# Optimization experiments

Hardware: AMD Instinct MI355X
Metric: run time of the kernel (lower is better)

Reference implementation:

```python
import jax, jax.numpy as jnp
import numpy as np

NUM_EXPERTS = 8
TOP_K = 2


def setup_inputs() -> dict:
    key = jax.random.key(0)
    k1, k2, k3, k4, k5 = jax.random.split(key, 5)
    B, S, H, F, E = 4, 2048, 1024, 4096, NUM_EXPERTS
    return {
        "hidden_states": jax.random.normal(k1, (B, S, H), dtype=jnp.float32),
        "gate_w": jax.random.normal(k2, (E, H), dtype=jnp.float32) * 0.02,
        "w1": jax.random.normal(k3, (E, F, H), dtype=jnp.float32) * 0.02,
        "w3": jax.random.normal(k4, (E, F, H), dtype=jnp.float32) * 0.02,
        "w2": jax.random.normal(k5, (E, H, F), dtype=jnp.float32) * 0.02,
    }


def reference(hidden_states, gate_w, w1, w3, w2):
    B, S, H = hidden_states.shape
    E = gate_w.shape[0]
    x = hidden_states.reshape(-1, H)  # [T, H]
    T = x.shape[0]

    # Router: logits -> fp32 softmax -> top-k -> renormalize (Mixtral)
    router_logits = x @ gate_w.T  # [T, E]
    probs = jax.nn.softmax(router_logits.astype(jnp.float32), axis=-1)
    top_w, top_idx = jax.lax.top_k(probs, TOP_K)  # [T, K]
    top_w = top_w / jnp.sum(top_w, axis=-1, keepdims=True)
    top_w = top_w.astype(x.dtype)

    # Combine weights per (token, expert); zero for unselected experts.
    comb = jnp.zeros((T, E), dtype=x.dtype).at[
        jnp.arange(T)[:, None], top_idx
    ].add(top_w)  # [T, E]

    out = jnp.zeros((T, H), dtype=x.dtype)
    for e in range(E):  # structural loop over distinct expert weights
        h = jax.nn.silu(x @ w1[e].T) * (x @ w3[e].T)  # [T, F]
        out = out + comb[:, e:e + 1] * (h @ w2[e].T)  # [T, H]

    return out.reshape(B, S, H), router_logits
```

## Files before the change

### kernel.cpp

```cpp
#include <hip/hip_runtime.h>
#include <hip/hip_bf16.h>
#include <stdint.h>

#define T_TOK 8192
#define H_DIM 1024
#define F_DIM 4096
#define NEXP  8
#define CAP        17408
#define CT128      136

typedef __attribute__((ext_vector_type(8))) short bf16x8;
typedef __attribute__((ext_vector_type(4))) float f32x4;

#define AS1 __attribute__((address_space(1)))
#define AS3 __attribute__((address_space(3)))

__device__ __forceinline__ void gload_lds16(const void* g, void* l) {
  __builtin_amdgcn_global_load_lds((const AS1 void*)g, (AS3 void*)l, 16, 0, 0);
}

__device__ __forceinline__ void nt_store_bf16(__hip_bfloat16* p, float v) {
  union { __hip_bfloat16 b; short s; } u; u.b = __float2bfloat16(v);
  __builtin_nontemporal_store(u.s, (short*)p);
}

struct TK { int i0, i1; float w0, w1; };

__global__ __launch_bounds__(256) void router_kernel(
    const float* __restrict__ x, const float* __restrict__ gw,
    float* __restrict__ logits, int* __restrict__ counts, TK* __restrict__ tk)
{
  const int lane = threadIdx.x & 63;
  const int t = blockIdx.x * 4 + (threadIdx.x >> 6);
  const float* xp = x + (size_t)t * H_DIM;
  float xr[16];
#pragma unroll
  for (int i = 0; i < 16; ++i) xr[i] = xp[lane + i * 64];
  float lg[NEXP];
#pragma unroll
  for (int e = 0; e < NEXP; ++e) {
    const float* gp = gw + e * H_DIM;
    float acc = 0.f;
#pragma unroll
    for (int i = 0; i < 16; ++i) acc += xr[i] * gp[lane + i * 64];
#pragma unroll
    for (int s = 32; s > 0; s >>= 1) acc += __shfl_xor(acc, s, 64);
    lg[e] = acc;
  }
  if (lane < NEXP) logits[(size_t)t * NEXP + lane] = lg[lane];
  if (lane == 0) {
    int i0 = 0; float m0 = lg[0];
#pragma unroll
    for (int e = 1; e < NEXP; ++e) if (lg[e] > m0) { m0 = lg[e]; i0 = e; }
    int i1 = -1; float m1 = -1e30f;
#pragma unroll
    for (int e = 0; e < NEXP; ++e) if (e != i0 && lg[e] > m1) { m1 = lg[e]; i1 = e; }
    float r = expf(m1 - m0);
    float w0 = 1.f / (1.f + r);
    float w1 = r / (1.f + r);
    TK v; v.i0 = i0; v.i1 = i1; v.w0 = w0; v.w1 = w1;
    tk[t] = v;
    atomicAdd(&counts[i0], 1);
    atomicAdd(&counts[i1], 1);
  }
}

__global__ __launch_bounds__(256) void scan_kernel(
    const int* __restrict__ counts, int* __restrict__ offs,
    int* __restrict__ cursor, int* __restrict__ tile_expert)
{
  __shared__ int so[NEXP + 1];
  const int tid = threadIdx.x;
  if (tid == 0) {
    int o = 0;
    for (int e = 0; e < NEXP; ++e) {
      so[e] = o; offs[e] = o; cursor[e] = o;
      o += (counts[e] + 127) & ~127;
    }
    so[NEXP] = o; offs[NEXP] = o;
  }
  __syncthreads();
  for (int ti = tid; ti < CT128; ti += 256) {
    int row = ti * 128;
    int e = NEXP - 1;
#pragma unroll
    for (int k = 0; k < NEXP; ++k)
      if (row >= so[k] && row < so[k + 1]) { e = k; break; }
    tile_expert[ti] = e;
  }
}

__global__ __launch_bounds__(256) void scatter_kernel(
    const TK* __restrict__ tk, int* __restrict__ cursor,
    int* __restrict__ pair_tok, float* __restrict__ pair_w,
    int2* __restrict__ inv)
{
  int t = blockIdx.x * 256 + threadIdx.x;
  if (t >= T_TOK) return;
  TK v = tk[t];
  int p0 = atomicAdd(&cursor[v.i0], 1);
  pair_tok[p0] = t; pair_w[p0] = v.w0;
  int p1 = atomicAdd(&cursor[v.i1], 1);
  pair_tok[p1] = t; pair_w[p1] = v.w1;
  inv[t] = make_int2(p0, p1);
}

union Pack8 { __hip_bfloat16 o[8]; uint4 u; };

__global__ __launch_bounds__(256) void gather_kernel(
    const float* __restrict__ x, const int* __restrict__ pair_tok,
    __hip_bfloat16* __restrict__ xg)
{
  int idx = blockIdx.x * 256 + threadIdx.x;
  int row = idx >> 7;
  int c8  = (idx & 127) << 3;
  int tok = pair_tok[row];
  const float4* src = reinterpret_cast<const float4*>(x + (size_t)tok * H_DIM + c8);
  float4 a = src[0], b = src[1];
  Pack8 pk;
  pk.o[0] = __float2bfloat16(a.x); pk.o[1] = __float2bfloat16(a.y);
  pk.o[2] = __float2bfloat16(a.z); pk.o[3] = __float2bfloat16(a.w);
  pk.o[4] = __float2bfloat16(b.x); pk.o[5] = __float2bfloat16(b.y);
  pk.o[6] = __float2bfloat16(b.z); pk.o[7] = __float2bfloat16(b.w);
  *reinterpret_cast<uint4*>(xg + (size_t)row * H_DIM + c8) = pk.u;
}

__global__ __launch_bounds__(256) void convert_kernel(
    const float* __restrict__ src, __hip_bfloat16* __restrict__ dst, long long n)
{
  long long i = ((long long)blockIdx.x * 256 + threadIdx.x) * 8;
  if (i >= n) return;
  float4 a = *reinterpret_cast<const float4*>(src + i);
  float4 b = *reinterpret_cast<const float4*>(src + i + 4);
  Pack8 pk;
  pk.o[0] = __float2bfloat16(a.x); pk.o[1] = __float2bfloat16(a.y);
  pk.o[2] = __float2bfloat16(a.z); pk.o[3] = __float2bfloat16(a.w);
  pk.o[4] = __float2bfloat16(b.x); pk.o[5] = __float2bfloat16(b.y);
  pk.o[6] = __float2bfloat16(b.z); pk.o[7] = __float2bfloat16(b.w);
  *reinterpret_cast<uint4*>(dst + i) = pk.u;
}


__global__ __launch_bounds__(256, 3) void gemm1_kernel(
    const __hip_bfloat16* __restrict__ xg,
    const __hip_bfloat16* __restrict__ w1b,
    const __hip_bfloat16* __restrict__ w3b,
    const int* __restrict__ tile_expert,
    __hip_bfloat16* __restrict__ h)
{
  __shared__ __hip_bfloat16 sA[128 * 64], sB1[64 * 64], sB3[64 * 64];
  const int n_  = blockIdx.x;
  const int idx = (n_ & 7) * 1088 + (n_ >> 3);
  const int tm  = idx % 136;
  const int tf  = idx / 136;
  const int e   = tile_expert[tm];
  const int tid = threadIdx.x;

  const __hip_bfloat16* A  = xg  + (size_t)tm * 128 * H_DIM;
  const __hip_bfloat16* B1 = w1b + (size_t)e * F_DIM * H_DIM + (size_t)tf * 64 * H_DIM;
  const __hip_bfloat16* B3 = w3b + (size_t)e * F_DIM * H_DIM + (size_t)tf * 64 * H_DIM;

  const int rs  = tid >> 3;
  const int sl  = tid & 7;
  const int xsl = (sl ^ (rs & 7)) * 8;
  const int dst = rs * 64 + sl * 8;

  const int wv = tid >> 6, lane = tid & 63;
  const int wm = wv >> 1, wn = wv & 1;
  const int l16 = lane & 15, lk = lane >> 4;
  const int ps0 = ((0 + lk) ^ (l16 & 7)) * 8;
  const int ps1 = ((4 + lk) ^ (l16 & 7)) * 8;

  f32x4 acc1[4][2] = {};
  f32x4 acc3[4][2] = {};

  for (int kt = 0; kt < H_DIM / 64; ++kt) {
    __syncthreads();
    const int gk = kt * 64 + xsl;
#pragma unroll
    for (int c = 0; c < 4; ++c)
      gload_lds16(A + (size_t)(rs + 32 * c) * H_DIM + gk, &sA[c * 2048 + dst]);
#pragma unroll
    for (int c = 0; c < 2; ++c) {
      gload_lds16(B1 + (size_t)(rs + 32 * c) * H_DIM + gk, &sB1[c * 2048 + dst]);
      gload_lds16(B3 + (size_t)(rs + 32 * c) * H_DIM + gk, &sB3[c * 2048 + dst]);
    }
    __syncthreads();
#pragma unroll
    for (int ks = 0; ks < 2; ++ks) {
      const int ps = ks ? ps1 : ps0;
      bf16x8 a[4], b1[2], b3[2];
#pragma unroll
      for (int m = 0; m < 4; ++m)
        a[m] = *reinterpret_cast<const bf16x8*>(&sA[(wm * 64 + m * 16 + l16) * 64 + ps]);
#pragma unroll
      for (int nf = 0; nf < 2; ++nf) {
        b1[nf] = *reinterpret_cast<const bf16x8*>(&sB1[(wn * 32 + nf * 16 + l16) * 64 + ps]);
        b3[nf] = *reinterpret_cast<const bf16x8*>(&sB3[(wn * 32 + nf * 16 + l16) * 64 + ps]);
      }
#pragma unroll
      for (int m = 0; m < 4; ++m)
#pragma unroll
        for (int nf = 0; nf < 2; ++nf) {
          acc1[m][nf] = __builtin_amdgcn_mfma_f32_16x16x32_bf16(a[m], b1[nf], acc1[m][nf], 0, 0, 0);
          acc3[m][nf] = __builtin_amdgcn_mfma_f32_16x16x32_bf16(a[m], b3[nf], acc3[m][nf], 0, 0, 0);
        }
    }
  }

  __hip_bfloat16* hp = h + (size_t)tm * 128 * F_DIM + (size_t)tf * 64;
#pragma unroll
  for (int m = 0; m < 4; ++m)
#pragma unroll
    for (int nf = 0; nf < 2; ++nf)
#pragma unroll
      for (int j = 0; j < 4; ++j) {
        int row = wm * 64 + m * 16 + lk * 4 + j;
        int col = wn * 32 + nf * 16 + l16;
        float c1 = acc1[m][nf][j];
        float c3 = acc3[m][nf][j];
        float s  = c1 / (1.f + expf(-c1));
        nt_store_bf16(&hp[(size_t)row * F_DIM + col], s * c3);
      }
}

__global__ __launch_bounds__(256, 3) void gemm2_kernel(
    const __hip_bfloat16* __restrict__ h,
    const __hip_bfloat16* __restrict__ w2b,
    const int* __restrict__ tile_expert,
    const float* __restrict__ pair_w,
    float* __restrict__ y)
{
  __shared__ __hip_bfloat16 sA[128 * 64], sB[128 * 64];
  const int n_  = blockIdx.x;
  const int idx = (n_ & 7) * 136 + (n_ >> 3);
  const int tm  = idx % 136;
  const int tn  = idx / 136;
  const int e   = tile_expert[tm];
  const int tid = threadIdx.x;

  const __hip_bfloat16* A = h   + (size_t)tm * 128 * F_DIM;
  const __hip_bfloat16* B = w2b + (size_t)e * H_DIM * F_DIM + (size_t)tn * 128 * F_DIM;

  const int rs  = tid >> 3;
  const int sl  = tid & 7;
  const int xsl = (sl ^ (rs & 7)) * 8;
  const int dst = rs * 64 + sl * 8;

  const int wv = tid >> 6, lane = tid & 63;
  const int wm = wv >> 1, wn = wv & 1;
  const int l16 = lane & 15, lk = lane >> 4;
  const int ps0 = ((0 + lk) ^ (l16 & 7)) * 8;
  const int ps1 = ((4 + lk) ^ (l16 & 7)) * 8;

  f32x4 acc[4][4] = {};

  for (int kt = 0; kt < F_DIM / 64; ++kt) {
    __syncthreads();
    const int gk = kt * 64 + xsl;
#pragma unroll
    for (int c = 0; c < 4; ++c) {
      gload_lds16(A + (size_t)(rs + 32 * c) * F_DIM + gk, &sA[c * 2048 + dst]);
      gload_lds16(B + (size_t)(rs + 32 * c) * F_DIM + gk, &sB[c * 2048 + dst]);
    }
    __syncthreads();
#pragma unroll
    for (int ks = 0; ks < 2; ++ks) {
      const int ps = ks ? ps1 : ps0;
      bf16x8 a[4], b[4];
#pragma unroll
      for (int m = 0; m < 4; ++m)
        a[m] = *reinterpret_cast<const bf16x8*>(&sA[(wm * 64 + m * 16 + l16) * 64 + ps]);
#pragma unroll
      for (int nf = 0; nf < 4; ++nf)
        b[nf] = *reinterpret_cast<const bf16x8*>(&sB[(wn * 64 + nf * 16 + l16) * 64 + ps]);
#pragma unroll
      for (int m = 0; m < 4; ++m)
#pragma unroll
        for (int nf = 0; nf < 4; ++nf)
          acc[m][nf] = __builtin_amdgcn_mfma_f32_16x16x32_bf16(a[m], b[nf], acc[m][nf], 0, 0, 0);
    }
  }

#pragma unroll
  for (int m = 0; m < 4; ++m)
#pragma unroll
    for (int j = 0; j < 4; ++j) {
      int rowg = tm * 128 + wm * 64 + m * 16 + lk * 4 + j;
      float w = pair_w[rowg];
      float* op = y + (size_t)rowg * H_DIM + tn * 128 + wn * 64;
#pragma unroll
      for (int nf = 0; nf < 4; ++nf)
        __builtin_nontemporal_store(w * acc[m][nf][j], op + nf * 16 + l16);
    }
}

__global__ __launch_bounds__(256) void combine_kernel(
    const float* __restrict__ y, const int2* __restrict__ inv,
    float* __restrict__ out)
{
  int idx = blockIdx.x * 256 + threadIdx.x;
  int t  = idx >> 8;
  int c  = (idx & 255) << 2;
  int2 p = inv[t];
  float4 a = *reinterpret_cast<const float4*>(y + (size_t)p.x * H_DIM + c);
  float4 b = *reinterpret_cast<const float4*>(y + (size_t)p.y * H_DIM + c);
  float4 o; o.x = a.x + b.x; o.y = a.y + b.y; o.z = a.z + b.z; o.w = a.w + b.w;
  *reinterpret_cast<float4*>(out + (size_t)t * H_DIM + c) = o;
}

#define WS_COUNTS   0
#define WS_CURSOR   32
#define WS_OFFS     64
#define WS_TILEEXP  128
#define WS_TK       1024
#define WS_PAIRTOK  132096
#define WS_PAIRW    201728
#define WS_ZERO_BYTES 271360
#define WS_INV      271360
#define WS_XG       336896ll
#define WS_W1       (WS_XG + 35651584ll)
#define WS_W3       (WS_W1 + 67108864ll)
#define WS_W2       (WS_W3 + 67108864ll)
#define WS_H        (WS_W2 + 67108864ll)
#define WS_Y        WS_XG

extern "C" void kernel_launch(void* const* d_in, const int* in_sizes, int n_in,
                              void* d_out, int out_size, void* d_ws, size_t ws_size,
                              hipStream_t stream) {
  const float* x  = (const float*)d_in[0];
  const float* gw = (const float*)d_in[1];
  const float* w1 = (const float*)d_in[2];
  const float* w3 = (const float*)d_in[3];
  const float* w2 = (const float*)d_in[4];
  float* out    = (float*)d_out;
  float* logits = out + (size_t)T_TOK * H_DIM;

  char* ws = (char*)d_ws;
  int*   counts   = (int*)(ws + WS_COUNTS);
  int*   cursor   = (int*)(ws + WS_CURSOR);
  int*   offs     = (int*)(ws + WS_OFFS);
  int*   tile_exp = (int*)(ws + WS_TILEEXP);
  TK*    tk       = (TK*)(ws + WS_TK);
  int*   pair_tok = (int*)(ws + WS_PAIRTOK);
  float* pair_w   = (float*)(ws + WS_PAIRW);
  int2*  inv      = (int2*)(ws + WS_INV);
  __hip_bfloat16* xg  = (__hip_bfloat16*)(ws + WS_XG);
  __hip_bfloat16* w1b = (__hip_bfloat16*)(ws + WS_W1);
  __hip_bfloat16* w3b = (__hip_bfloat16*)(ws + WS_W3);
  __hip_bfloat16* w2b = (__hip_bfloat16*)(ws + WS_W2);
  __hip_bfloat16* hbuf = (__hip_bfloat16*)(ws + WS_H);
  float* ybuf = (float*)(ws + WS_Y);

  hipMemsetAsync(d_ws, 0, WS_ZERO_BYTES, stream);

  const long long nW = (long long)NEXP * F_DIM * H_DIM;
  convert_kernel<<<16384, 256, 0, stream>>>(w1, w1b, nW);
  convert_kernel<<<16384, 256, 0, stream>>>(w3, w3b, nW);
  convert_kernel<<<16384, 256, 0, stream>>>(w2, w2b, nW);

  router_kernel<<<T_TOK / 4, 256, 0, stream>>>(x, gw, logits, counts, tk);
  scan_kernel<<<1, 256, 0, stream>>>(counts, offs, cursor, tile_exp);
  scatter_kernel<<<T_TOK / 256, 256, 0, stream>>>(tk, cursor, pair_tok, pair_w, inv);
  gather_kernel<<<(CAP * 128) / 256, 256, 0, stream>>>(x, pair_tok, xg);

  gemm1_kernel<<<CT128 * (F_DIM / 64), 256, 0, stream>>>(
      xg, w1b, w3b, tile_exp, hbuf);
  gemm2_kernel<<<CT128 * (H_DIM / 128), 256, 0, stream>>>(
      hbuf, w2b, tile_exp, pair_w, ybuf);
  combine_kernel<<<(T_TOK * H_DIM / 4) / 256, 256, 0, stream>>>(ybuf, inv, out);
}
```

Measured before the change: 974.6 us.

## Stage GEMM epilogues through LDS and store expert outputs in bf16

Both GEMM epilogues now write results into shared memory first, then copy them out with coalesced 16-byte vector stores instead of scattered scalar nontemporal stores. The per-pair expert output buffer y changes from fp32 to bf16, which halves the bytes written by gemm2 and read by the combine kernel; the combine kernel is rewritten to read 8 bf16 values per thread. The gemm1 tile mapping also changes so the F tiles vary fastest within a token tile, which alters cache reuse. In exchange, y is rounded to bf16, adding some precision loss before the final sum.

```diff
diff --git a/kernel.cpp b/kernel.cpp
--- a/kernel.cpp
+++ b/kernel.cpp
@@ -17,11 +17,6 @@
 
 __device__ __forceinline__ void gload_lds16(const void* g, void* l) {
   __builtin_amdgcn_global_load_lds((const AS1 void*)g, (AS3 void*)l, 16, 0, 0);
-}
-
-__device__ __forceinline__ void nt_store_bf16(__hip_bfloat16* p, float v) {
-  union { __hip_bfloat16 b; short s; } u; u.b = __float2bfloat16(v);
-  __builtin_nontemporal_store(u.s, (short*)p);
 }
 
 struct TK { int i0, i1; float w0, w1; };
@@ -148,11 +143,15 @@
     const int* __restrict__ tile_expert,
     __hip_bfloat16* __restrict__ h)
 {
-  __shared__ __hip_bfloat16 sA[128 * 64], sB1[64 * 64], sB3[64 * 64];
+  __shared__ __hip_bfloat16 smem[16384];
+  __hip_bfloat16* sA  = smem;
+  __hip_bfloat16* sB1 = smem + 8192;
+  __hip_bfloat16* sB3 = smem + 12288;
+
   const int n_  = blockIdx.x;
   const int idx = (n_ & 7) * 1088 + (n_ >> 3);
-  const int tm  = idx % 136;
-  const int tf  = idx / 136;
+  const int tm  = idx >> 6;
+  const int tf  = idx & 63;
   const int e   = tile_expert[tm];
   const int tid = threadIdx.x;
 
@@ -208,7 +207,7 @@
     }
   }
 
-  __hip_bfloat16* hp = h + (size_t)tm * 128 * F_DIM + (size_t)tf * 64;
+  __syncthreads();
 #pragma unroll
   for (int m = 0; m < 4; ++m)
 #pragma unroll
@@ -220,8 +219,17 @@
         float c1 = acc1[m][nf][j];
         float c3 = acc3[m][nf][j];
         float s  = c1 / (1.f + expf(-c1));
-        nt_store_bf16(&hp[(size_t)row * F_DIM + col], s * c3);
+        smem[row * 64 + col] = __float2bfloat16(s * c3);
       }
+  __syncthreads();
+  const uint4* s4 = reinterpret_cast<const uint4*>(smem);
+  __hip_bfloat16* hp = h + (size_t)tm * 128 * F_DIM + (size_t)tf * 64;
+#pragma unroll
+  for (int i = 0; i < 4; ++i) {
+    int c = i * 256 + tid;
+    int row = c >> 3, sg = c & 7;
+    *reinterpret_cast<uint4*>(hp + (size_t)row * F_DIM + sg * 8) = s4[c];
+  }
 }
 
 __global__ __launch_bounds__(256, 3) void gemm2_kernel(
@@ -229,9 +237,12 @@
     const __hip_bfloat16* __restrict__ w2b,
     const int* __restrict__ tile_expert,
     const float* __restrict__ pair_w,
-    float* __restrict__ y)
-{
-  __shared__ __hip_bfloat16 sA[128 * 64], sB[128 * 64];
+    __hip_bfloat16* __restrict__ y)
+{
+  __shared__ __hip_bfloat16 smem[16384];
+  __hip_bfloat16* sA = smem;
+  __hip_bfloat16* sB = smem + 8192;
+
   const int n_  = blockIdx.x;
   const int idx = (n_ & 7) * 136 + (n_ >> 3);
   const int tm  = idx % 136;
@@ -282,31 +293,53 @@
     }
   }
 
+  __syncthreads();
 #pragma unroll
   for (int m = 0; m < 4; ++m)
 #pragma unroll
     for (int j = 0; j < 4; ++j) {
-      int rowg = tm * 128 + wm * 64 + m * 16 + lk * 4 + j;
-      float w = pair_w[rowg];
-      float* op = y + (size_t)rowg * H_DIM + tn * 128 + wn * 64;
-#pragma unroll
-      for (int nf = 0; nf < 4; ++nf)
-        __builtin_nontemporal_store(w * acc[m][nf][j], op + nf * 16 + l16);
-    }
+      int row  = wm * 64 + m * 16 + lk * 4 + j;
+      float w  = pair_w[tm * 128 + row];
+#pragma unroll
+      for (int nf = 0; nf < 4; ++nf) {
+        int col = wn * 64 + nf * 16 + l16;
+        smem[row * 128 + col] = __float2bfloat16(w * acc[m][nf][j]);
+      }
+    }
+  __syncthreads();
+  const uint4* s4 = reinterpret_cast<const uint4*>(smem);
+  __hip_bfloat16* yp = y + (size_t)tm * 128 * H_DIM + (size_t)tn * 128;
+#pragma unroll
+  for (int i = 0; i < 8; ++i) {
+    int c = i * 256 + tid;
+    int row = c >> 4, sg = c & 15;
+    *reinterpret_cast<uint4*>(yp + (size_t)row * H_DIM + sg * 8) = s4[c];
+  }
 }
 
 __global__ __launch_bounds__(256) void combine_kernel(
-    const float* __restrict__ y, const int2* __restrict__ inv,
+    const __hip_bfloat16* __restrict__ y, const int2* __restrict__ inv,
     float* __restrict__ out)
 {
   int idx = blockIdx.x * 256 + threadIdx.x;
-  int t  = idx >> 8;
-  int c  = (idx & 255) << 2;
+  int t  = idx >> 7;
+  int c8 = (idx & 127) << 3;
   int2 p = inv[t];
-  float4 a = *reinterpret_cast<const float4*>(y + (size_t)p.x * H_DIM + c);
-  float4 b = *reinterpret_cast<const float4*>(y + (size_t)p.y * H_DIM + c);
-  float4 o; o.x = a.x + b.x; o.y = a.y + b.y; o.z = a.z + b.z; o.w = a.w + b.w;
-  *reinterpret_cast<float4*>(out + (size_t)t * H_DIM + c) = o;
+  union { uint4 u; __hip_bfloat16 o[8]; } a, b;
+  a.u = *reinterpret_cast<const uint4*>(y + (size_t)p.x * H_DIM + c8);
+  b.u = *reinterpret_cast<const uint4*>(y + (size_t)p.y * H_DIM + c8);
+  float4 o0, o1;
+  o0.x = __bfloat162float(a.o[0]) + __bfloat162float(b.o[0]);
+  o0.y = __bfloat162float(a.o[1]) + __bfloat162float(b.o[1]);
+  o0.z = __bfloat162float(a.o[2]) + __bfloat162float(b.o[2]);
+  o0.w = __bfloat162float(a.o[3]) + __bfloat162float(b.o[3]);
+  o1.x = __bfloat162float(a.o[4]) + __bfloat162float(b.o[4]);
+  o1.y = __bfloat162float(a.o[5]) + __bfloat162float(b.o[5]);
+  o1.z = __bfloat162float(a.o[6]) + __bfloat162float(b.o[6]);
+  o1.w = __bfloat162float(a.o[7]) + __bfloat162float(b.o[7]);
+  float* op = out + (size_t)t * H_DIM + c8;
+  *reinterpret_cast<float4*>(op)     = o0;
+  *reinterpret_cast<float4*>(op + 4) = o1;
 }
 
 #define WS_COUNTS   0
@@ -350,7 +383,7 @@
   __hip_bfloat16* w3b = (__hip_bfloat16*)(ws + WS_W3);
   __hip_bfloat16* w2b = (__hip_bfloat16*)(ws + WS_W2);
   __hip_bfloat16* hbuf = (__hip_bfloat16*)(ws + WS_H);
-  float* ybuf = (float*)(ws + WS_Y);
+  __hip_bfloat16* ybuf = (__hip_bfloat16*)(ws + WS_Y);
 
   hipMemsetAsync(d_ws, 0, WS_ZERO_BYTES, stream);
 
@@ -368,5 +401,5 @@
       xg, w1b, w3b, tile_exp, hbuf);
   gemm2_kernel<<<CT128 * (H_DIM / 128), 256, 0, stream>>>(
       hbuf, w2b, tile_exp, pair_w, ybuf);
-  combine_kernel<<<(T_TOK * H_DIM / 4) / 256, 256, 0, stream>>>(ybuf, inv, out);
-}
+  combine_kernel<<<(T_TOK * H_DIM / 8) / 256, 256, 0, stream>>>(ybuf, inv, out);
+}
```

Measured after the change: 938.9 us. -3.7%, faster.
